# Kernel tuning notes

Hardware: AMD Instinct MI355X
Metric: run time of the kernel (lower is better)

Reference implementation:

```python
import jax, jax.numpy as jnp
import numpy as np

N_NODES = 20000
N_EDGES = 320000
T = 8
C_IN = 32
C_OUT = 32
C_EDGE = 16


def setup_inputs() -> dict:
    key = jax.random.key(0)
    ks = jax.random.split(key, 10)

    def xavier(k, shape):
        fan_in, fan_out = shape[0], shape[1]
        limit = float(np.sqrt(6.0 / (fan_in + fan_out)))
        return jax.random.uniform(k, shape, jnp.float32, -limit, limit)

    X = jax.random.normal(ks[0], (N_NODES, T, C_IN), jnp.float32)
    edge_index = jax.random.randint(ks[1], (2, N_EDGES), 0, N_NODES, jnp.int32)
    edge_attr = jax.random.normal(ks[2], (N_EDGES, C_EDGE), jnp.float32)
    Wn1 = xavier(ks[3], (C_IN, C_OUT))
    We1 = xavier(ks[4], (C_EDGE, C_OUT))
    u1 = xavier(ks[5], (C_OUT, C_OUT))
    Wn2 = xavier(ks[6], (C_OUT, C_OUT))
    We2 = xavier(ks[7], (C_EDGE, C_OUT))
    u2 = xavier(ks[8], (C_OUT, C_OUT))
    return {"X": X, "edge_index": edge_index, "edge_attr": edge_attr,
            "Wn1": Wn1, "We1": We1, "u1": u1,
            "Wn2": Wn2, "We2": We2, "u2": u2}


def _gat_conv(x, edge_index, edge_attr, Wn, We, u):
    # x: [N, T, C_in] -> h: [N, T, C_out]
    h = jnp.matmul(x, Wn)
    _ea = jnp.matmul(edge_attr, We)  # computed in original forward, unused in message (dead code)
    # per-edge matmul with u == node-level matmul then gather (same math, cheaper)
    hu = jnp.matmul(h, u)  # [N, T, C]
    src, tgt = edge_index[0], edge_index[1]
    x_j = hu[src]  # [E, T, C]
    x_i = hu[tgt]  # [E, T, C]
    gate = jax.nn.sigmoid(jnp.sum(x_i * x_j, axis=-1, keepdims=True))  # [E, T, 1]
    msg = x_j * gate  # [E, T, C]
    agg = jax.ops.segment_max(msg, tgt, num_segments=N_NODES)  # max-aggregate into targets
    agg = jnp.where(jnp.isfinite(agg), agg, jnp.zeros((), agg.dtype))  # empty segments -> 0 (PyG fill)
    return h + agg  # residual update


def reference(X, edge_index, edge_attr, Wn1, We1, u1, Wn2, We2, u2):
    c1 = jax.nn.leaky_relu(_gat_conv(X, edge_index, edge_attr, Wn1, We1, u1), 0.01)
    c2 = jax.nn.leaky_relu(_gat_conv(c1, edge_index, edge_attr, Wn2, We2, u2), 0.01)
    return c2
```

## Files before the change

kernel.cpp:

```cpp
#include <hip/hip_runtime.h>
#include <hip/hip_fp16.h>
#include <cstdint>
#include <cstddef>
#include <math.h>

#define NNODES 20000
#define NEDGES 320000
#define TDIM   8
#define CDIM   32
#define RROWS  (NNODES * TDIM)
#define NELEM  (RROWS * CDIM)

static __device__ __forceinline__ unsigned pk2(float a, float b) {
    __half2 h = __floats2half2_rn(a, b);
    return *reinterpret_cast<unsigned*>(&h);
}

static __device__ __forceinline__ void cvt8(uint4 r, float* a) {
    float2 f;
    f = __half22float2(*reinterpret_cast<__half2*>(&r.x)); a[0] = f.x; a[1] = f.y;
    f = __half22float2(*reinterpret_cast<__half2*>(&r.y)); a[2] = f.x; a[3] = f.y;
    f = __half22float2(*reinterpret_cast<__half2*>(&r.z)); a[4] = f.x; a[5] = f.y;
    f = __half22float2(*reinterpret_cast<__half2*>(&r.w)); a[6] = f.x; a[7] = f.y;
}

__global__ __launch_bounds__(1024) void wu_kernel(
    const float* __restrict__ W1, const float* __restrict__ U1, float* __restrict__ WU1,
    const float* __restrict__ W2, const float* __restrict__ U2, float* __restrict__ WU2)
{
    const float* W  = blockIdx.x ? W2  : W1;
    const float* U  = blockIdx.x ? U2  : U1;
    float*       WU = blockIdx.x ? WU2 : WU1;
    int t = threadIdx.x;
    int k = t >> 5, c = t & 31;
    float acc = 0.f;
#pragma unroll
    for (int j = 0; j < CDIM; ++j) acc = fmaf(W[k * CDIM + j], U[j * CDIM + c], acc);
    WU[k * CDIM + c] = acc;
}

__global__ __launch_bounds__(256) void linear2_kernel(
    const float* __restrict__ in,
    const float* __restrict__ W,
    const float* __restrict__ WU,
    float* __restrict__ h,
    __half* __restrict__ hu16)
{
    __shared__ float sx[64][33];
    int tid = threadIdx.x;
    int rowBase = blockIdx.x * 64;

    const float4* in4 = (const float4*)(in + (size_t)rowBase * CDIM);
#pragma unroll
    for (int i = 0; i < 2; ++i) {
        int idx = tid + i * 256;
        float4 v = in4[idx];
        int r = idx >> 3, q = idx & 7;
        sx[r][4 * q + 0] = v.x; sx[r][4 * q + 1] = v.y;
        sx[r][4 * q + 2] = v.z; sx[r][4 * q + 3] = v.w;
    }
    __syncthreads();

    int lane  = tid & 63;
    int chunk = __builtin_amdgcn_readfirstlane(tid >> 6);
    int row = rowBase + lane;

    float hr[8], acc[8];
#pragma unroll
    for (int j = 0; j < 8; ++j) { hr[j] = 0.f; acc[j] = 0.f; }

    const float* Wc  = W  + chunk * 8;
    const float* WUc = WU + chunk * 8;
#pragma unroll 4
    for (int k = 0; k < CDIM; ++k) {
        float xk = sx[lane][k];
#pragma unroll
        for (int j = 0; j < 8; ++j) {
            hr[j]  = fmaf(xk, Wc[k * CDIM + j],  hr[j]);
            acc[j] = fmaf(xk, WUc[k * CDIM + j], acc[j]);
        }
    }

    float* hp = h + (size_t)row * CDIM + chunk * 8;
    ((float4*)hp)[0] = make_float4(hr[0], hr[1], hr[2], hr[3]);
    ((float4*)hp)[1] = make_float4(hr[4], hr[5], hr[6], hr[7]);

    uint4* up = (uint4*)((char*)hu16 + (size_t)row * 64 + chunk * 16);
    *up = make_uint4(pk2(acc[0], acc[1]), pk2(acc[2], acc[3]),
                     pk2(acc[4], acc[5]), pk2(acc[6], acc[7]));
}

__global__ __launch_bounds__(256) void zero_counts_kernel(int* __restrict__ counts)
{
    int i = blockIdx.x * 256 + threadIdx.x;
    if (i < NNODES) counts[i] = 0;
}

__global__ __launch_bounds__(256) void hist_kernel(
    const int* __restrict__ ei, int* __restrict__ counts)
{
    int e = blockIdx.x * 256 + threadIdx.x;
    if (e < NEDGES) atomicAdd(&counts[ei[NEDGES + e]], 1);
}

__global__ __launch_bounds__(256) void blocksum_kernel(
    const int* __restrict__ counts, int* __restrict__ bsum)
{
    __shared__ int sd[256];
    int tid = threadIdx.x;
    int i = blockIdx.x * 256 + tid;
    sd[tid] = (i < NNODES) ? counts[i] : 0;
    __syncthreads();
#pragma unroll
    for (int off = 128; off > 0; off >>= 1) {
        if (tid < off) sd[tid] += sd[tid + off];
        __syncthreads();
    }
    if (tid == 0) bsum[blockIdx.x] = sd[0];
}

__global__ __launch_bounds__(128) void bscan_kernel(
    const int* __restrict__ bsum, int* __restrict__ bbase, int nblocks)
{
    __shared__ int sd[128];
    int tid = threadIdx.x;
    int v = (tid < nblocks) ? bsum[tid] : 0;
    sd[tid] = v;
    __syncthreads();
#pragma unroll
    for (int off = 1; off < 128; off <<= 1) {
        int t = (tid >= off) ? sd[tid - off] : 0;
        __syncthreads();
        sd[tid] += t;
        __syncthreads();
    }
    if (tid < nblocks) bbase[tid] = sd[tid] - v;
}

__global__ __launch_bounds__(256) void localscan_kernel(
    const int* __restrict__ counts, const int* __restrict__ bbase,
    int* __restrict__ offsets, int* __restrict__ cursor)
{
    __shared__ int sd[256];
    int tid = threadIdx.x;
    int i = blockIdx.x * 256 + tid;
    int v = (i < NNODES) ? counts[i] : 0;
    sd[tid] = v;
    __syncthreads();
#pragma unroll
    for (int off = 1; off < 256; off <<= 1) {
        int t = (tid >= off) ? sd[tid - off] : 0;
        __syncthreads();
        sd[tid] += t;
        __syncthreads();
    }
    int excl = bbase[blockIdx.x] + sd[tid] - v;
    if (i < NNODES) { offsets[i] = excl; cursor[i] = excl; }
    if (i == NNODES - 1) offsets[NNODES] = NEDGES;
}

__global__ __launch_bounds__(256) void scatter_kernel(
    const int* __restrict__ ei,
    int* __restrict__ cursor,
    int* __restrict__ csr_src)
{
    int e = blockIdx.x * 256 + threadIdx.x;
    if (e < NEDGES) {
        int t = ei[NEDGES + e];
        int pos = atomicAdd(&cursor[t], 1);
        csr_src[pos] = ei[e];
    }
}

__global__ __launch_bounds__(256) void agg_kernel(
    const int* __restrict__ offsets,
    const int* __restrict__ csr_src,
    const __half* __restrict__ hu16,
    const float* h,
    float* out)
{
    int tid = threadIdx.x;
    int n = blockIdx.x * 4 + (tid >> 6);
    int l64 = tid & 63;
    int half = l64 >> 5;
    int l32 = l64 & 31;
    uint32_t rowOff = (uint32_t)l32 * 16u;
    const char* hub = (const char*)hu16;

    float b[8];
    cvt8(*(const uint4*)(hub + ((uint32_t)n << 9) + rowOff), b);

    int k0 = offsets[n];
    int k1 = offsets[n + 1];

    float m[8];
#pragma unroll
    for (int j = 0; j < 8; ++j) m[j] = -INFINITY;

    int k = k0;
    int e0 = 0, e1 = 0;
    if (k + 4 <= k1) {
        e0 = csr_src[k + half];
        e1 = csr_src[k + 2 + half];
    }
    while (k + 4 <= k1) {
        uint4 r0 = *(const uint4*)(hub + (((uint32_t)e0 << 9) + rowOff));
        uint4 r1 = *(const uint4*)(hub + (((uint32_t)e1 << 9) + rowOff));
        k += 4;
        if (k + 4 <= k1) {
            e0 = csr_src[k + half];
            e1 = csr_src[k + 2 + half];
        }
        float a0[8], a1[8];
        cvt8(r0, a0); cvt8(r1, a1);
        float q0 = 0.f, q1 = 0.f;
#pragma unroll
        for (int j = 0; j < 8; ++j) { q0 = fmaf(a0[j], b[j], q0); q1 = fmaf(a1[j], b[j], q1); }
        q0 += __shfl_xor(q0, 1); q1 += __shfl_xor(q1, 1);
        q0 += __shfl_xor(q0, 2); q1 += __shfl_xor(q1, 2);
        float g0 = 1.f / (1.f + __expf(-q0));
        float g1 = 1.f / (1.f + __expf(-q1));
#pragma unroll
        for (int j = 0; j < 8; ++j) {
            m[j] = fmaxf(m[j], a0[j] * g0);
            m[j] = fmaxf(m[j], a1[j] * g1);
        }
    }
    for (; k < k1; ++k) {
        int s = csr_src[k];
        float a0[8];
        cvt8(*(const uint4*)(hub + (((uint32_t)s << 9) + rowOff)), a0);
        float q0 = 0.f;
#pragma unroll
        for (int j = 0; j < 8; ++j) q0 = fmaf(a0[j], b[j], q0);
        q0 += __shfl_xor(q0, 1);
        q0 += __shfl_xor(q0, 2);
        float g0 = 1.f / (1.f + __expf(-q0));
#pragma unroll
        for (int j = 0; j < 8; ++j) m[j] = fmaxf(m[j], a0[j] * g0);
    }

#pragma unroll
    for (int j = 0; j < 8; ++j) m[j] = fmaxf(m[j], __shfl_xor(m[j], 32));

    if (half == 0) {
        bool has = (k1 > k0);
        uint32_t nodeOff = (uint32_t)n * 1024u + (uint32_t)l32 * 32u;
        const char* hb = (const char*)h;
        float4 hv0 = *(const float4*)(hb + nodeOff);
        float4 hv1 = *(const float4*)(hb + nodeOff + 16);
        float o[8];
        float hvv[8] = {hv0.x, hv0.y, hv0.z, hv0.w, hv1.x, hv1.y, hv1.z, hv1.w};
#pragma unroll
        for (int j = 0; j < 8; ++j) {
            float a = has ? m[j] : 0.f;
            float vv = hvv[j] + a;
            o[j] = (vv >= 0.f) ? vv : 0.01f * vv;
        }
        char* ob = (char*)out;
        *(float4*)(ob + nodeOff)      = make_float4(o[0], o[1], o[2], o[3]);
        *(float4*)(ob + nodeOff + 16) = make_float4(o[4], o[5], o[6], o[7]);
    }
}

extern "C" void kernel_launch(void* const* d_in, const int* in_sizes, int n_in,
                              void* d_out, int out_size, void* d_ws, size_t ws_size,
                              hipStream_t stream)
{
    const float* X   = (const float*)d_in[0];
    const int*   ei  = (const int*)  d_in[1];
    const float* Wn1 = (const float*)d_in[3];
    const float* u1  = (const float*)d_in[5];
    const float* Wn2 = (const float*)d_in[6];
    const float* u2  = (const float*)d_in[8];

    float* out = (float*)d_out;

    int* counts  = (int*)d_ws;
    int* offsets = counts + NNODES;
    int* cursor  = offsets + NNODES + 1;
    int* bsum    = cursor + NNODES;
    int* bbase   = bsum + 128;
    float* WU1   = (float*)(bbase + 128);
    float* WU2   = WU1 + 1024;
    int* csr     = (int*)(WU2 + 1024);
    float*  A   = (float*)(((uintptr_t)(csr + NEDGES) + 255) & ~(uintptr_t)255);
    __half* H16 = (__half*)(A + NELEM);

    const int linBlocks  = RROWS / 64;
    const int edgeBlocks = (NEDGES + 255) / 256;
    const int nodeBlocks = (NNODES + 255) / 256;
    const int aggBlocks  = NNODES / 4;

    wu_kernel<<<2, 1024, 0, stream>>>(Wn1, u1, WU1, Wn2, u2, WU2);
    zero_counts_kernel<<<nodeBlocks, 256, 0, stream>>>(counts);
    hist_kernel<<<edgeBlocks, 256, 0, stream>>>(ei, counts);
    blocksum_kernel<<<nodeBlocks, 256, 0, stream>>>(counts, bsum);
    bscan_kernel<<<1, 128, 0, stream>>>(bsum, bbase, nodeBlocks);
    localscan_kernel<<<nodeBlocks, 256, 0, stream>>>(counts, bbase, offsets, cursor);
    scatter_kernel<<<edgeBlocks, 256, 0, stream>>>(ei, cursor, csr);

    linear2_kernel<<<linBlocks, 256, 0, stream>>>(X, Wn1, WU1, A, H16);
    agg_kernel<<<aggBlocks, 256, 0, stream>>>(offsets, csr, H16, A, A);

    linear2_kernel<<<linBlocks, 256, 0, stream>>>(A, Wn2, WU2, out, H16);
    agg_kernel<<<aggBlocks, 256, 0, stream>>>(offsets, csr, H16, out, out);
}
```

Measured before the change: 145.9 us.

## Store intermediate h and layer-1 output in fp16 and merge preprocessing kernels

The residual tensor h and the layer-1 activation are now stored in half precision, which halves the bytes written and read between the linear and aggregation stages. The zeroing and weight-product kernels are merged into one launch. The three-kernel scan is replaced by a single scan kernel in which each block recomputes its prefix by summing all earlier counts. This cuts the launch count, but the residual path loses precision and later scan blocks do redundant summing work.

```diff
diff --git a/kernel.cpp b/kernel.cpp
--- a/kernel.cpp
+++ b/kernel.cpp
@@ -10,6 +10,7 @@
 #define CDIM   32
 #define RROWS  (NNODES * TDIM)
 #define NELEM  (RROWS * CDIM)
+#define NODEB  79
 
 static __device__ __forceinline__ unsigned pk2(float a, float b) {
     __half2 h = __floats2half2_rn(a, b);
@@ -24,40 +25,114 @@
     f = __half22float2(*reinterpret_cast<__half2*>(&r.w)); a[6] = f.x; a[7] = f.y;
 }
 
-__global__ __launch_bounds__(1024) void wu_kernel(
-    const float* __restrict__ W1, const float* __restrict__ U1, float* __restrict__ WU1,
-    const float* __restrict__ W2, const float* __restrict__ U2, float* __restrict__ WU2)
-{
-    const float* W  = blockIdx.x ? W2  : W1;
-    const float* U  = blockIdx.x ? U2  : U1;
-    float*       WU = blockIdx.x ? WU2 : WU1;
-    int t = threadIdx.x;
-    int k = t >> 5, c = t & 31;
+__global__ __launch_bounds__(256) void init_kernel(
+    const float* __restrict__ Wn1, const float* __restrict__ u1, float* __restrict__ WU1,
+    const float* __restrict__ Wn2, const float* __restrict__ u2, float* __restrict__ WU2,
+    int* __restrict__ counts)
+{
+    int blk = blockIdx.x, tid = threadIdx.x;
+    if (blk < NODEB) {
+        int i = blk * 256 + tid;
+        if (i < NNODES) counts[i] = 0;
+        return;
+    }
+    int b = blk - NODEB;
+    const float* W  = (b < 4) ? Wn1 : Wn2;
+    const float* U  = (b < 4) ? u1  : u2;
+    float*       WU = (b < 4) ? WU1 : WU2;
+    int idx = (b & 3) * 256 + tid;
+    int k = idx >> 5, c = idx & 31;
     float acc = 0.f;
 #pragma unroll
     for (int j = 0; j < CDIM; ++j) acc = fmaf(W[k * CDIM + j], U[j * CDIM + c], acc);
-    WU[k * CDIM + c] = acc;
-}
-
+    WU[idx] = acc;
+}
+
+__global__ __launch_bounds__(256) void hist_kernel(
+    const int* __restrict__ ei, int* __restrict__ counts)
+{
+    int e = blockIdx.x * 256 + threadIdx.x;
+    if (e < NEDGES) atomicAdd(&counts[ei[NEDGES + e]], 1);
+}
+
+__global__ __launch_bounds__(256) void scan_kernel(
+    const int* __restrict__ counts,
+    int* __restrict__ offsets, int* __restrict__ cursor)
+{
+    __shared__ int sd[256];
+    int blk = blockIdx.x, tid = threadIdx.x;
+
+    int pre = 0;
+    for (int i = tid; i < blk * 256; i += 256) pre += counts[i];
+    sd[tid] = pre;
+    __syncthreads();
+#pragma unroll
+    for (int off = 128; off > 0; off >>= 1) {
+        if (tid < off) sd[tid] += sd[tid + off];
+        __syncthreads();
+    }
+    int base = sd[0];
+    __syncthreads();
+
+    int i = blk * 256 + tid;
+    int v = (i < NNODES) ? counts[i] : 0;
+    sd[tid] = v;
+    __syncthreads();
+#pragma unroll
+    for (int off = 1; off < 256; off <<= 1) {
+        int t = (tid >= off) ? sd[tid - off] : 0;
+        __syncthreads();
+        sd[tid] += t;
+        __syncthreads();
+    }
+    int excl = base + sd[tid] - v;
+    if (i < NNODES) { offsets[i] = excl; cursor[i] = excl; }
+    if (i == NNODES - 1) offsets[NNODES] = NEDGES;
+}
+
+__global__ __launch_bounds__(256) void scatter_kernel(
+    const int* __restrict__ ei,
+    int* __restrict__ cursor,
+    int* __restrict__ csr_src)
+{
+    int e = blockIdx.x * 256 + threadIdx.x;
+    if (e < NEDGES) {
+        int t = ei[NEDGES + e];
+        int pos = atomicAdd(&cursor[t], 1);
+        csr_src[pos] = ei[e];
+    }
+}
+
+template<bool IN16>
 __global__ __launch_bounds__(256) void linear2_kernel(
-    const float* __restrict__ in,
+    const void* __restrict__ inp,
     const float* __restrict__ W,
     const float* __restrict__ WU,
-    float* __restrict__ h,
+    __half* __restrict__ h16,
     __half* __restrict__ hu16)
 {
     __shared__ float sx[64][33];
     int tid = threadIdx.x;
     int rowBase = blockIdx.x * 64;
 
-    const float4* in4 = (const float4*)(in + (size_t)rowBase * CDIM);
-#pragma unroll
-    for (int i = 0; i < 2; ++i) {
-        int idx = tid + i * 256;
-        float4 v = in4[idx];
-        int r = idx >> 3, q = idx & 7;
-        sx[r][4 * q + 0] = v.x; sx[r][4 * q + 1] = v.y;
-        sx[r][4 * q + 2] = v.z; sx[r][4 * q + 3] = v.w;
+    if (IN16) {
+        const char* base = (const char*)inp + (size_t)rowBase * 64;
+        uint4 v = *(const uint4*)(base + (size_t)tid * 16);
+        float a[8];
+        cvt8(v, a);
+        int r = tid >> 2, q = tid & 3;
+#pragma unroll
+        for (int j = 0; j < 8; ++j) sx[r][q * 8 + j] = a[j];
+    } else {
+        const float4* in4 = (const float4*)((const float*)inp + (size_t)rowBase * CDIM);
+#pragma unroll
+        for (int i = 0; i < 2; ++i) {
+            int idx = tid + i * 256;
+            float4 v = in4[idx];
+            int r = idx >> 3, q = idx & 7;
+            sx[r][4 * q + 0] = v.x; sx[r][4 * q + 1] = v.y;
+            sx[r][4 * q + 2] = v.z; sx[r][4 * q + 3] = v.w;
+        }
     }
     __syncthreads();
 
@@ -81,103 +156,22 @@
         }
     }
 
-    float* hp = h + (size_t)row * CDIM + chunk * 8;
-    ((float4*)hp)[0] = make_float4(hr[0], hr[1], hr[2], hr[3]);
-    ((float4*)hp)[1] = make_float4(hr[4], hr[5], hr[6], hr[7]);
+    uint4* hp = (uint4*)((char*)h16 + (size_t)row * 64 + chunk * 16);
+    *hp = make_uint4(pk2(hr[0], hr[1]), pk2(hr[2], hr[3]),
+                     pk2(hr[4], hr[5]), pk2(hr[6], hr[7]));
 
     uint4* up = (uint4*)((char*)hu16 + (size_t)row * 64 + chunk * 16);
     *up = make_uint4(pk2(acc[0], acc[1]), pk2(acc[2], acc[3]),
                      pk2(acc[4], acc[5]), pk2(acc[6], acc[7]));
 }
 
-__global__ __launch_bounds__(256) void zero_counts_kernel(int* __restrict__ counts)
-{
-    int i = blockIdx.x * 256 + threadIdx.x;
-    if (i < NNODES) counts[i] = 0;
-}
-
-__global__ __launch_bounds__(256) void hist_kernel(
-    const int* __restrict__ ei, int* __restrict__ counts)
-{
-    int e = blockIdx.x * 256 + threadIdx.x;
-    if (e < NEDGES) atomicAdd(&counts[ei[NEDGES + e]], 1);
-}
-
-__global__ __launch_bounds__(256) void blocksum_kernel(
-    const int* __restrict__ counts, int* __restrict__ bsum)
-{
-    __shared__ int sd[256];
-    int tid = threadIdx.x;
-    int i = blockIdx.x * 256 + tid;
-    sd[tid] = (i < NNODES) ? counts[i] : 0;
-    __syncthreads();
-#pragma unroll
-    for (int off = 128; off > 0; off >>= 1) {
-        if (tid < off) sd[tid] += sd[tid + off];
-        __syncthreads();
-    }
-    if (tid == 0) bsum[blockIdx.x] = sd[0];
-}
-
-__global__ __launch_bounds__(128) void bscan_kernel(
-    const int* __restrict__ bsum, int* __restrict__ bbase, int nblocks)
-{
-    __shared__ int sd[128];
-    int tid = threadIdx.x;
-    int v = (tid < nblocks) ? bsum[tid] : 0;
-    sd[tid] = v;
-    __syncthreads();
-#pragma unroll
-    for (int off = 1; off < 128; off <<= 1) {
-        int t = (tid >= off) ? sd[tid - off] : 0;
-        __syncthreads();
-        sd[tid] += t;
-        __syncthreads();
-    }
-    if (tid < nblocks) bbase[tid] = sd[tid] - v;
-}
-
-__global__ __launch_bounds__(256) void localscan_kernel(
-    const int* __restrict__ counts, const int* __restrict__ bbase,
-    int* __restrict__ offsets, int* __restrict__ cursor)
-{
-    __shared__ int sd[256];
-    int tid = threadIdx.x;
-    int i = blockIdx.x * 256 + tid;
-    int v = (i < NNODES) ? counts[i] : 0;
-    sd[tid] = v;
-    __syncthreads();
-#pragma unroll
-    for (int off = 1; off < 256; off <<= 1) {
-        int t = (tid >= off) ? sd[tid - off] : 0;
-        __syncthreads();
-        sd[tid] += t;
-        __syncthreads();
-    }
-    int excl = bbase[blockIdx.x] + sd[tid] - v;
-    if (i < NNODES) { offsets[i] = excl; cursor[i] = excl; }
-    if (i == NNODES - 1) offsets[NNODES] = NEDGES;
-}
-
-__global__ __launch_bounds__(256) void scatter_kernel(
-    const int* __restrict__ ei,
-    int* __restrict__ cursor,
-    int* __restrict__ csr_src)
-{
-    int e = blockIdx.x * 256 + threadIdx.x;
-    if (e < NEDGES) {
-        int t = ei[NEDGES + e];
-        int pos = atomicAdd(&cursor[t], 1);
-        csr_src[pos] = ei[e];
-    }
-}
-
+template<bool OUT16>
 __global__ __launch_bounds__(256) void agg_kernel(
     const int* __restrict__ offsets,
     const int* __restrict__ csr_src,
     const __half* __restrict__ hu16,
-    const float* h,
-    float* out)
+    const __half* __restrict__ h16,
+    void* __restrict__ outp)
 {
     int tid = threadIdx.x;
     int n = blockIdx.x * 4 + (tid >> 6);
@@ -245,21 +239,25 @@
 
     if (half == 0) {
         bool has = (k1 > k0);
-        uint32_t nodeOff = (uint32_t)n * 1024u + (uint32_t)l32 * 32u;
-        const char* hb = (const char*)h;
-        float4 hv0 = *(const float4*)(hb + nodeOff);
-        float4 hv1 = *(const float4*)(hb + nodeOff + 16);
+        float hv[8];
+        cvt8(*(const uint4*)((const char*)h16 + ((uint32_t)n << 9) + rowOff), hv);
         float o[8];
-        float hvv[8] = {hv0.x, hv0.y, hv0.z, hv0.w, hv1.x, hv1.y, hv1.z, hv1.w};
 #pragma unroll
         for (int j = 0; j < 8; ++j) {
             float a = has ? m[j] : 0.f;
-            float vv = hvv[j] + a;
+            float vv = hv[j] + a;
             o[j] = (vv >= 0.f) ? vv : 0.01f * vv;
         }
-        char* ob = (char*)out;
-        *(float4*)(ob + nodeOff)      = make_float4(o[0], o[1], o[2], o[3]);
-        *(float4*)(ob + nodeOff + 16) = make_float4(o[4], o[5], o[6], o[7]);
+        if (OUT16) {
+            uint4 w = make_uint4(pk2(o[0], o[1]), pk2(o[2], o[3]),
+                                 pk2(o[4], o[5]), pk2(o[6], o[7]));
+            *(uint4*)((char*)outp + ((uint32_t)n << 9) + rowOff) = w;
+        } else {
+            uint32_t nodeOff = (uint32_t)n * 1024u + (uint32_t)l32 * 32u;
+            char* ob = (char*)outp;
+            *(float4*)(ob + nodeOff)      = make_float4(o[0], o[1], o[2], o[3]);
+            *(float4*)(ob + nodeOff + 16) = make_float4(o[4], o[5], o[6], o[7]);
+        }
     }
 }
 
@@ -274,35 +272,28 @@
     const float* Wn2 = (const float*)d_in[6];
     const float* u2  = (const float*)d_in[8];
 
-    float* out = (float*)d_out;
-
     int* counts  = (int*)d_ws;
     int* offsets = counts + NNODES;
     int* cursor  = offsets + NNODES + 1;
-    int* bsum    = cursor + NNODES;
-    int* bbase   = bsum + 128;
-    float* WU1   = (float*)(bbase + 128);
+    float* WU1   = (float*)(cursor + NNODES);
     float* WU2   = WU1 + 1024;
     int* csr     = (int*)(WU2 + 1024);
-    float*  A   = (float*)(((uintptr_t)(csr + NEDGES) + 255) & ~(uintptr_t)255);
-    __half* H16 = (__half*)(A + NELEM);
+    __half* A16  = (__half*)(((uintptr_t)(csr + NEDGES) + 255) & ~(uintptr_t)255);
+    __half* Hh   = A16 + NELEM;
+    __half* HU   = Hh + NELEM;
 
     const int linBlocks  = RROWS / 64;
     const int edgeBlocks = (NEDGES + 255) / 256;
-    const int nodeBlocks = (NNODES + 255) / 256;
     const int aggBlocks  = NNODES / 4;
 
-    wu_kernel<<<2, 1024, 0, stream>>>(Wn1, u1, WU1, Wn2, u2, WU2);
-    zero_counts_kernel<<<nodeBlocks, 256, 0, stream>>>(counts);
+    init_kernel<<<NODEB + 8, 256, 0, stream>>>(Wn1, u1, WU1, Wn2, u2, WU2, counts);
     hist_kernel<<<edgeBlocks, 256, 0, stream>>>(ei, counts);
-    blocksum_kernel<<<nodeBlocks, 256, 0, stream>>>(counts, bsum);
-    bscan_kernel<<<1, 128, 0, stream>>>(bsum, bbase, nodeBlocks);
-    localscan_kernel<<<nodeBlocks, 256, 0, stream>>>(counts, bbase, offsets, cursor);
+    scan_kernel<<<NODEB, 256, 0, stream>>>(counts, offsets, cursor);
     scatter_kernel<<<edgeBlocks, 256, 0, stream>>>(ei, cursor, csr);
 
-    linear2_kernel<<<linBlocks, 256, 0, stream>>>(X, Wn1, WU1, A, H16);
-    agg_kernel<<<aggBlocks, 256, 0, stream>>>(offsets, csr, H16, A, A);
-
-    linear2_kernel<<<linBlocks, 256, 0, stream>>>(A, Wn2, WU2, out, H16);
-    agg_kernel<<<aggBlocks, 256, 0, stream>>>(offsets, csr, H16, out, out);
-}
+    linear2_kernel<false><<<linBlocks, 256, 0, stream>>>(X, Wn1, WU1, Hh, HU);
+    agg_kernel<true><<<aggBlocks, 256, 0, stream>>>(offsets, csr, HU, Hh, A16);
+
+    linear2_kernel<true><<<linBlocks, 256, 0, stream>>>(A16, Wn2, WU2, Hh, HU);
+    agg_kernel<false><<<aggBlocks, 256, 0, stream>>>(offsets, csr, HU, Hh, d_out);
+}
```

Measured after the change: 145.0 us. About the same (-0.6%).
